# Optimization experiments

Measured on AMD Instinct MI355X. Metric: run time of the kernel, lower is better.

## Reference

```python
import jax, jax.numpy as jnp
import numpy as np

S, B, D_IN, HID, N_HEADS = 512, 64, 256, 512, 4


def setup_inputs() -> dict:
    key = jax.random.key(0)
    ks = jax.random.split(key, 16)
    din = D_IN + HID  # 768, gate linear fan-in
    sg = 1.0 / np.sqrt(din)
    sa = 1.0 / np.sqrt(HID)
    n = lambda k, shape, s: (jax.random.normal(k, shape, jnp.float32) * s)
    return {
        "x": jax.random.normal(ks[0], (S, B, D_IN), jnp.float32),
        # LSTM gate weights, stored (in, out) for x @ W + b
        "Wf": n(ks[1], (din, HID), sg), "bf": n(ks[2], (HID,), sg),
        "Wi": n(ks[3], (din, HID), sg), "bi": n(ks[4], (HID,), sg),
        "Wg": n(ks[5], (din, HID), sg), "bg": n(ks[6], (HID,), sg),
        "Wo": n(ks[7], (din, HID), sg), "bo": n(ks[8], (HID,), sg),
        # attention projections (out_proj unused in original forward, omitted)
        "Wq": n(ks[9], (HID, HID), sa), "bq": n(ks[10], (HID,), sa),
        "Wk": n(ks[11], (HID, HID), sa), "bk": n(ks[12], (HID,), sa),
        "Wv": n(ks[13], (HID, HID), sa), "bv": n(ks[14], (HID,), sa),
    }


def _forward(x, Wf, bf, Wi, bi, Wg, bg, Wo, bo, Wq, bq, Wk, bk, Wv, bv):
    Sl, Bs, _ = x.shape
    h0 = jnp.zeros((Bs, HID), x.dtype)
    c0 = jnp.zeros((Bs, HID), x.dtype)

    def step(carry, xt):
        hx, cx = carry
        comb = jnp.concatenate([xt, hx], axis=1)  # [B, D_IN+HID]
        f = jax.nn.sigmoid(comb @ Wf + bf)
        i = jax.nn.sigmoid(comb @ Wi + bi)
        g = jnp.tanh(comb @ Wg + bg)
        o = jax.nn.sigmoid(comb @ Wo + bo)
        cx = f * cx + i * g
        hx = o * jnp.tanh(cx)
        return (hx, cx), hx

    (hx, cx), lstm_out = jax.lax.scan(step, (h0, c0), x)  # lstm_out: [S, B, HID]

    dk = HID // N_HEADS
    # Faithful to original quirk: view (S,B,E) linear output as (B,S,H,dk) without transposing
    def proj(W, b):
        return (lstm_out @ W + b).reshape(Bs, Sl, N_HEADS, dk).transpose(0, 2, 1, 3)

    q, k, v = proj(Wq, bq), proj(Wk, bk), proj(Wv, bv)  # [B, H, S, dk]
    scores = jnp.einsum('bhqd,bhkd->bhqk', q, k) / np.sqrt(dk)
    attn = jax.nn.softmax(scores, axis=-1)
    out = jnp.einsum('bhqk,bhkd->bhqd', attn, v)  # [B, H, S, dk]
    out = out.transpose(0, 2, 1, 3).reshape(Bs, Sl, HID)
    decoded = jnp.swapaxes(out, 0, 1)  # [S, B, HID]
    return decoded, hx, cx


def reference(x, Wf, bf, Wi, bi, Wg, bg, Wo, bo, Wq, bq, Wk, bk, Wv, bv):
    return _forward(x, Wf, bf, Wi, bi, Wg, bg, Wo, bo, Wq, bq, Wk, bk, Wv, bv)
```

## Files before the change

### kernel.cpp

```cpp
#include <hip/hip_runtime.h>
#include <hip/hip_bf16.h>

typedef __attribute__((ext_vector_type(8))) short s8;
typedef __attribute__((ext_vector_type(4))) float f4;

using bf16 = __hip_bfloat16;

#define MFMA16(a,b,c) __builtin_amdgcn_mfma_f32_16x16x32_bf16((a),(b),(c),0,0,0)

constexpr int SS = 512, BBATCH = 64, HIDN = 512;
constexpr size_t DEC_SZ = (size_t)SS * BBATCH * HIDN;

constexpr size_t OF_FLAGS = 0;
constexpr size_t OF_BIAS4 = 65536;
constexpr size_t OF_BIASQ = 73728;
constexpr size_t OF_BTX   = 131072;
constexpr size_t OF_BTH   = 1179648;
constexpr size_t OF_BTQKV = 3276800;
constexpr size_t OF_YQ    = (size_t)5  << 20;
constexpr size_t OF_YK    = OF_YQ + ((size_t)32 << 20);
constexpr size_t OF_VT    = OF_YK + ((size_t)32 << 20);

constexpr size_t DOUT_LOUT = 0;
constexpr size_t DOUT_XBF  = (size_t)32 << 20;

__device__ inline s8 ldg8(const bf16* p){ return *(const s8*)p; }
__device__ inline short f2bs(float f){ return __builtin_bit_cast(short, __float2bfloat16(f)); }
__device__ inline float sigf(float x){ return 1.f/(1.f + __expf(-x)); }
__device__ inline float tanhf_(float x){ x = fminf(fmaxf(x, -15.f), 15.f); float e = __expf(2.f*x); return (e-1.f)/(e+1.f); }

__global__ void k0_pack(const float* x,
                        const float* Wf,const float* Wi,const float* Wg,const float* Wo,
                        const float* bfv,const float* biv,const float* bgv,const float* bov,
                        const float* Wq,const float* Wk,const float* Wv,
                        const float* bqv,const float* bkv,const float* bvv,
                        bf16* xbf, bf16* btx, bf16* bth, bf16* btqkv,
                        float* bias4, float* biasq, int* flags)
{
  const float* WG[4] = {Wf, Wi, Wg, Wo};
  const float* BG[4] = {bfv, biv, bgv, bov};
  const float* WQ[3] = {Wq, Wk, Wv};
  const float* BQ[3] = {bqv, bkv, bvv};
  const long NX   = 8388608;
  const long NBTH = 1048576;
  const long NBTQ = 786432;
  const long NBTX = 524288;
  const long NF   = 16384;
  const long TOT  = NX + NBTH + NBTQ + NBTX + NF + 2048 + 1536;
  long stride = (long)gridDim.x * blockDim.x;
  for (long i = (long)blockIdx.x*blockDim.x + threadIdx.x; i < TOT; i += stride){
    if (i < NX){ xbf[i] = __float2bfloat16(x[i]); }
    else if (i < NX + NBTH){
      long j = i - NX; int n = (int)(j >> 9), k = (int)(j & 511);
      int g = n >> 9, hid = n & 511;
      bth[j] = __float2bfloat16(WG[g][(size_t)(256 + k)*512 + hid]);
    } else if (i < NX + NBTH + NBTQ){
      long j = i - NX - NBTH; int n = (int)(j >> 9), k = (int)(j & 511);
      int w = n >> 9, c = n & 511;
      btqkv[j] = __float2bfloat16(WQ[w][(size_t)k*512 + c]);
    } else if (i < NX + NBTH + NBTQ + NBTX){
      long j = i - NX - NBTH - NBTQ; int n = (int)(j >> 8), k = (int)(j & 255);
      int g = n >> 9, hid = n & 511;
      btx[j] = __float2bfloat16(WG[g][(size_t)k*512 + hid]);
    } else if (i < NX + NBTH + NBTQ + NBTX + NF){
      flags[i - NX - NBTH - NBTQ - NBTX] = 0;
    } else if (i < NX + NBTH + NBTQ + NBTX + NF + 2048){
      long j = i - NX - NBTH - NBTQ - NBTX - NF; int g = (int)(j >> 9), hid = (int)(j & 511);
      bias4[j] = BG[g][hid];
    } else {
      long j = i - NX - NBTH - NBTQ - NBTX - NF - 2048; int w = (int)(j >> 9), c = (int)(j & 511);
      biasq[j] = BQ[w][c];
    }
  }
}

__global__ __launch_bounds__(512) void k1_lstm(const bf16* xbf, const bf16* btx, const bf16* bth,
                                               const float* bias4, bf16* lout, int* flags,
                                               float* out_tail)
{
  int ns = blockIdx.x;
  int tid = threadIdx.x, w = tid >> 6, lane = tid & 63;
  int mt = w >> 1, nh = w & 1, lm = lane & 15, q = lane >> 4;
  __shared__ float pre[64][68];
  s8 Bh[2][16], Bx[2][8];
  #pragma unroll
  for (int i = 0; i < 2; ++i){
    const bf16* bph = bth + ((size_t)((2*nh+i)*512 + ns*16 + lm)) * 512;
    #pragma unroll
    for (int kk = 0; kk < 16; ++kk) Bh[i][kk] = ldg8(bph + kk*32 + q*8);
    const bf16* bpx = btx + ((size_t)((2*nh+i)*512 + ns*16 + lm)) * 256;
    #pragma unroll
    for (int kk = 0; kk < 8; ++kk) Bx[i][kk] = ldg8(bpx + kk*32 + q*8);
  }
  int c0 = 2*tid, b0 = c0 >> 4, j0 = c0 & 15;
  float bs[8];
  #pragma unroll
  for (int g = 0; g < 4; ++g){
    bs[g]   = bias4[g*512 + ns*16 + j0];
    bs[4+g] = bias4[g*512 + ns*16 + j0 + 1];
  }
  float cs0 = 0.f, cs1 = 0.f;
  int budget = 1 << 22;

  for (int t = 0; t < 512; ++t){
    f4 acc[2] = {{0,0,0,0},{0,0,0,0}};
    const bf16* xr = xbf + ((size_t)(t*64 + mt*16 + lm)) * 256;
    #pragma unroll
    for (int kk = 0; kk < 8; ++kk){
      s8 A = ldg8(xr + kk*32 + q*8);
      acc[0] = MFMA16(A, Bx[0][kk], acc[0]);
      acc[1] = MFMA16(A, Bx[1][kk], acc[1]);
    }
    if (t > 0){
      int* fb = flags + (size_t)(t-1)*32;
      while (budget > 0){
        int v = 1;
        if (lane < 32) v = __hip_atomic_load(fb + lane, __ATOMIC_RELAXED, __HIP_MEMORY_SCOPE_AGENT);
        if (__ballot(v != 0) == ~0ull) break;
        budget--;
        __builtin_amdgcn_s_sleep(1);
      }
      __builtin_amdgcn_fence(__ATOMIC_ACQUIRE, "agent");
      const bf16* hr = lout + ((size_t)((t-1)*64 + mt*16 + lm)) * 512;
      #pragma unroll
      for (int kk = 0; kk < 16; ++kk){
        s8 A = ldg8(hr + kk*32 + q*8);
        acc[0] = MFMA16(A, Bh[0][kk], acc[0]);
        acc[1] = MFMA16(A, Bh[1][kk], acc[1]);
      }
    }
    #pragma unroll
    for (int i = 0; i < 2; ++i){
      int col = (2*nh+i)*16 + lm;
      #pragma unroll
      for (int r = 0; r < 4; ++r) pre[mt*16 + q*4 + r][col] = acc[i][r];
    }
    __syncthreads();
    {
      float fh0 = pre[b0][ 0+j0] + bs[0], fh1 = pre[b0][ 0+j0+1] + bs[4];
      float ih0 = pre[b0][16+j0] + bs[1], ih1 = pre[b0][16+j0+1] + bs[5];
      float gh0 = pre[b0][32+j0] + bs[2], gh1 = pre[b0][32+j0+1] + bs[6];
      float oh0 = pre[b0][48+j0] + bs[3], oh1 = pre[b0][48+j0+1] + bs[7];
      cs0 = sigf(fh0)*cs0 + sigf(ih0)*tanhf_(gh0);
      cs1 = sigf(fh1)*cs1 + sigf(ih1)*tanhf_(gh1);
      float h0 = sigf(oh0)*tanhf_(cs0);
      float h1 = sigf(oh1)*tanhf_(cs1);
      unsigned hv = (unsigned)(unsigned short)f2bs(h0) | ((unsigned)(unsigned short)f2bs(h1) << 16);
      __hip_atomic_store((unsigned*)(lout + ((size_t)(t*64 + b0))*512 + ns*16 + j0),
                         hv, __ATOMIC_RELAXED, __HIP_MEMORY_SCOPE_AGENT);
      if (t == 511){
        float* hx = out_tail + (size_t)b0*512 + ns*16 + j0;
        hx[0] = h0; hx[1] = h1;
        float* cx = out_tail + 32768 + (size_t)b0*512 + ns*16 + j0;
        cx[0] = cs0; cx[1] = cs1;
      }
    }
    __syncthreads();
    if (tid == 0)
      __hip_atomic_store(flags + (size_t)t*32 + ns, 1, __ATOMIC_RELEASE, __HIP_MEMORY_SCOPE_AGENT);
  }
}

__global__ __launch_bounds__(512) void k2_qkv(const bf16* lout, const bf16* btqkv, const float* biasq,
                                              bf16* yq, bf16* yk, bf16* vt)
{
  int nb = blockIdx.x, rb = blockIdx.y;
  int tid = threadIdx.x, w = tid >> 6, lane = tid & 63;
  int mt = w >> 1, nh = w & 1, lm = lane & 15, q = lane >> 4;
  int row = rb*64 + mt*16 + lm;
  f4 acc[2] = {{0,0,0,0},{0,0,0,0}};
  const bf16* ap  = lout + (size_t)row * 512;
  const bf16* bp0 = btqkv + ((size_t)(nb*64 + (2*nh+0)*16 + lm)) * 512;
  const bf16* bp1 = btqkv + ((size_t)(nb*64 + (2*nh+1)*16 + lm)) * 512;
  #pragma unroll
  for (int kk = 0; kk < 16; ++kk){
    int kb = kk*32 + q*8;
    s8 A = ldg8(ap + kb);
    acc[0] = MFMA16(A, ldg8(bp0 + kb), acc[0]);
    acc[1] = MFMA16(A, ldg8(bp1 + kb), acc[1]);
  }
  #pragma unroll
  for (int i = 0; i < 2; ++i){
    int e = nb*64 + (2*nh+i)*16 + lm;
    float bias = biasq[e];
    #pragma unroll
    for (int r = 0; r < 4; ++r){
      int rr = rb*64 + mt*16 + q*4 + r;
      bf16 v = __float2bfloat16(acc[i][r] + bias);
      if (e < 512)        yq[(size_t)rr*512 + e] = v;
      else if (e < 1024)  yk[(size_t)rr*512 + (e-512)] = v;
      else {
        int d = e - 1024, hh = d >> 7, dh = d & 127;
        vt[((size_t)((rr >> 9)*4 + hh)*128 + dh)*512 + (rr & 511)] = v;
      }
    }
  }
}

__global__ __launch_bounds__(256) void k3_attn(const bf16* yq, const bf16* yk, const bf16* vt,
                                               float* dec)
{
  int rb = blockIdx.x, bh = blockIdx.y;
  int b1 = bh >> 2, hh = bh & 3;
  int tid = threadIdx.x, w = tid >> 6, lane = tid & 63, lm = lane & 15, q = lane >> 4;
  __shared__ short sbuf[32768];
  short (*sK)[128] = (short(*)[128])sbuf;
  s8 Af[4];
  const bf16* apr = yq + ((size_t)(b1*512 + rb*64 + w*16 + lm))*512 + hh*128;
  #pragma unroll
  for (int kk = 0; kk < 4; ++kk) Af[kk] = ldg8(apr + kk*32 + q*8);
  f4 acc[32];
  #pragma unroll
  for (int nt = 0; nt < 32; ++nt) acc[nt] = (f4){0,0,0,0};

  for (int ch = 0; ch < 4; ++ch){
    __syncthreads();
    #pragma unroll
    for (int it = 0; it < 8; ++it){
      int lin = tid + it*256;
      int srow = lin >> 4, seg = lin & 15;
      int pseg = seg ^ (srow & 15);
      *(s8*)&sK[srow][pseg*8] =
        ldg8(yk + ((size_t)(b1*512 + ch*128 + srow))*512 + hh*128 + seg*8);
    }
    __syncthreads();
    #pragma unroll
    for (int ntl = 0; ntl < 8; ++ntl){
      int nt = ch*8 + ntl;
      int brow = ntl*16 + lm;
      #pragma unroll
      for (int kk = 0; kk < 4; ++kk){
        int c = (kk*4 + q) ^ lm;
        s8 Bfr = *(const s8*)&sK[brow][c*8];
        acc[nt] = MFMA16(Af[kk], Bfr, acc[nt]);
      }
    }
  }
  const float scale = 0.08838834764831845f;
  float mx[4], sm[4];
  #pragma unroll
  for (int r = 0; r < 4; ++r){
    float m = -1e30f;
    #pragma unroll
    for (int nt = 0; nt < 32; ++nt) m = fmaxf(m, acc[nt][r]);
    mx[r] = m;
  }
  #pragma unroll
  for (int d = 1; d < 16; d <<= 1){
    #pragma unroll
    for (int r = 0; r < 4; ++r) mx[r] = fmaxf(mx[r], __shfl_xor(mx[r], d, 64));
  }
  #pragma unroll
  for (int r = 0; r < 4; ++r){
    float s = 0.f;
    #pragma unroll
    for (int nt = 0; nt < 32; ++nt){
      float e = __expf(scale * (acc[nt][r] - mx[r]));
      acc[nt][r] = e; s += e;
    }
    sm[r] = s;
  }
  #pragma unroll
  for (int d = 1; d < 16; d <<= 1){
    #pragma unroll
    for (int r = 0; r < 4; ++r) sm[r] += __shfl_xor(sm[r], d, 64);
  }
  float inv[4];
  #pragma unroll
  for (int r = 0; r < 4; ++r) inv[r] = 1.f / sm[r];

  __syncthreads();
  #pragma unroll
  for (int nt = 0; nt < 32; ++nt){
    #pragma unroll
    for (int r = 0; r < 4; ++r){
      int rowp = w*16 + q*4 + r, col = nt*16 + lm;
      sbuf[rowp*512 + (((col >> 3) ^ (rowp & 15))*8) + (col & 7)] =
        f2bs(acc[nt][r] * inv[r]);
    }
  }
  f4 o[8];
  #pragma unroll
  for (int n2 = 0; n2 < 8; ++n2) o[n2] = (f4){0,0,0,0};
  int rowa = w*16 + lm;
  #pragma unroll
  for (int kk = 0; kk < 16; ++kk){
    s8 A = *(const s8*)&sbuf[rowa*512 + (((kk*4 + q) ^ (rowa & 15))*8)];
    #pragma unroll
    for (int n2 = 0; n2 < 8; ++n2){
      s8 Bfr = ldg8(vt + ((size_t)(bh*128 + n2*16 + lm))*512 + kk*32 + q*8);
      o[n2] = MFMA16(A, Bfr, o[n2]);
    }
  }
  #pragma unroll
  for (int n2 = 0; n2 < 8; ++n2){
    int d = n2*16 + lm;
    #pragma unroll
    for (int r = 0; r < 4; ++r){
      int s1 = rb*64 + w*16 + q*4 + r;
      dec[((size_t)s1*64 + b1)*512 + hh*128 + d] = o[n2][r];
    }
  }
}

extern "C" void kernel_launch(void* const* d_in, const int* in_sizes, int n_in,
                              void* d_out, int out_size, void* d_ws, size_t ws_size,
                              hipStream_t stream)
{
  const float* x   = (const float*)d_in[0];
  const float* Wf  = (const float*)d_in[1];  const float* bfv = (const float*)d_in[2];
  const float* Wi  = (const float*)d_in[3];  const float* biv = (const float*)d_in[4];
  const float* Wg  = (const float*)d_in[5];  const float* bgv = (const float*)d_in[6];
  const float* Wo  = (const float*)d_in[7];  const float* bov = (const float*)d_in[8];
  const float* Wq  = (const float*)d_in[9];  const float* bqv = (const float*)d_in[10];
  const float* Wk  = (const float*)d_in[11]; const float* bkv = (const float*)d_in[12];
  const float* Wv  = (const float*)d_in[13]; const float* bvv = (const float*)d_in[14];

  char* ws = (char*)d_ws;
  int*   flags = (int*)  (ws + OF_FLAGS);
  float* bias4 = (float*)(ws + OF_BIAS4);
  float* biasq = (float*)(ws + OF_BIASQ);
  bf16*  btx   = (bf16*) (ws + OF_BTX);
  bf16*  bth   = (bf16*) (ws + OF_BTH);
  bf16*  btqkv = (bf16*) (ws + OF_BTQKV);
  bf16*  yq    = (bf16*) (ws + OF_YQ);
  bf16*  yk    = (bf16*) (ws + OF_YK);
  bf16*  vt    = (bf16*) (ws + OF_VT);

  char* outc = (char*)d_out;
  bf16*  lout = (bf16*)(outc + DOUT_LOUT);
  bf16*  xbf  = (bf16*)(outc + DOUT_XBF);
  float* out  = (float*)d_out;

  hipLaunchKernelGGL(k0_pack, dim3(2048), dim3(256), 0, stream,
                     x, Wf, Wi, Wg, Wo, bfv, biv, bgv, bov, Wq, Wk, Wv, bqv, bkv, bvv,
                     xbf, btx, bth, btqkv, bias4, biasq, flags);
  hipLaunchKernelGGL(k1_lstm, dim3(32), dim3(512), 0, stream,
                     xbf, btx, bth, bias4, lout, flags, out + DEC_SZ);
  hipLaunchKernelGGL(k2_qkv, dim3(24, 512), dim3(512), 0, stream, lout, btqkv, biasq, yq, yk, vt);
  hipLaunchKernelGGL(k3_attn, dim3(8, 256), dim3(256), 0, stream, yq, yk, vt, out);
}
```

Baseline: 4.996 ms.

## Pin LSTM recurrence blocks to a single XCD and relax cross-block sync

Launches 512 LSTM blocks but keeps only the 32 that land on XCC 0, handing out slice indices through an atomic claim counter. All cooperating blocks then share one L2, so flag polling uses sc0 loads, h and flag stores become plain or volatile stores, and the acquire fence drops to workgroup scope. This aims to cut the per-timestep cross-XCD coherence latency in the serial recurrence. It relies on the hardware XCC register and on same-XCD L2 coherence, and it spends launch overhead on blocks that exit immediately.

```diff
diff --git a/kernel.cpp b/kernel.cpp
--- a/kernel.cpp
+++ b/kernel.cpp
@@ -7,6 +7,8 @@
 using bf16 = __hip_bfloat16;
 
 #define MFMA16(a,b,c) __builtin_amdgcn_mfma_f32_16x16x32_bf16((a),(b),(c),0,0,0)
+
+#define GETREG_XCC_ID (20 | (0 << 6) | (3 << 11))
 
 constexpr int SS = 512, BBATCH = 64, HIDN = 512;
 constexpr size_t DEC_SZ = (size_t)SS * BBATCH * HIDN;
@@ -14,6 +16,7 @@
 constexpr size_t OF_FLAGS = 0;
 constexpr size_t OF_BIAS4 = 65536;
 constexpr size_t OF_BIASQ = 73728;
+constexpr size_t OF_CLAIM = 81920;
 constexpr size_t OF_BTX   = 131072;
 constexpr size_t OF_BTH   = 1179648;
 constexpr size_t OF_BTQKV = 3276800;
@@ -35,7 +38,7 @@
                         const float* Wq,const float* Wk,const float* Wv,
                         const float* bqv,const float* bkv,const float* bvv,
                         bf16* xbf, bf16* btx, bf16* bth, bf16* btqkv,
-                        float* bias4, float* biasq, int* flags)
+                        float* bias4, float* biasq, int* flags, int* claim)
 {
   const float* WG[4] = {Wf, Wi, Wg, Wo};
   const float* BG[4] = {bfv, biv, bgv, bov};
@@ -46,7 +49,7 @@
   const long NBTQ = 786432;
   const long NBTX = 524288;
   const long NF   = 16384;
-  const long TOT  = NX + NBTH + NBTQ + NBTX + NF + 2048 + 1536;
+  const long TOT  = NX + NBTH + NBTQ + NBTX + NF + 2048 + 1536 + 1;
   long stride = (long)gridDim.x * blockDim.x;
   for (long i = (long)blockIdx.x*blockDim.x + threadIdx.x; i < TOT; i += stride){
     if (i < NX){ xbf[i] = __float2bfloat16(x[i]); }
@@ -67,18 +70,33 @@
     } else if (i < NX + NBTH + NBTQ + NBTX + NF + 2048){
       long j = i - NX - NBTH - NBTQ - NBTX - NF; int g = (int)(j >> 9), hid = (int)(j & 511);
       bias4[j] = BG[g][hid];
-    } else {
+    } else if (i < NX + NBTH + NBTQ + NBTX + NF + 2048 + 1536){
       long j = i - NX - NBTH - NBTQ - NBTX - NF - 2048; int w = (int)(j >> 9), c = (int)(j & 511);
       biasq[j] = BQ[w][c];
+    } else {
+      claim[0] = 0;
     }
   }
 }
 
 __global__ __launch_bounds__(512) void k1_lstm(const bf16* xbf, const bf16* btx, const bf16* bth,
                                                const float* bias4, bf16* lout, int* flags,
-                                               float* out_tail)
-{
-  int ns = blockIdx.x;
+                                               int* claim, float* out_tail)
+{
+  __shared__ int s_ns;
+  int xcc = (int)(__builtin_amdgcn_s_getreg(GETREG_XCC_ID) & 15);
+  if (threadIdx.x == 0){
+    int nsl = -1;
+    if (xcc == 0){
+      nsl = __hip_atomic_fetch_add(claim, 1, __ATOMIC_RELAXED, __HIP_MEMORY_SCOPE_AGENT);
+      if (nsl >= 32) nsl = -1;
+    }
+    s_ns = nsl;
+  }
+  __syncthreads();
+  int ns = s_ns;
+  if (ns < 0) return;
+
   int tid = threadIdx.x, w = tid >> 6, lane = tid & 63;
   int mt = w >> 1, nh = w & 1, lm = lane & 15, q = lane >> 4;
   __shared__ float pre[64][68];
@@ -100,7 +118,7 @@
     bs[4+g] = bias4[g*512 + ns*16 + j0 + 1];
   }
   float cs0 = 0.f, cs1 = 0.f;
-  int budget = 1 << 22;
+  int budget = 1 << 20;
 
   for (int t = 0; t < 512; ++t){
     f4 acc[2] = {{0,0,0,0},{0,0,0,0}};
@@ -112,15 +130,16 @@
       acc[1] = MFMA16(A, Bx[1][kk], acc[1]);
     }
     if (t > 0){
-      int* fb = flags + (size_t)(t-1)*32;
+      const int* fp = flags + (size_t)(t-1)*32 + (lane & 31);
       while (budget > 0){
-        int v = 1;
-        if (lane < 32) v = __hip_atomic_load(fb + lane, __ATOMIC_RELAXED, __HIP_MEMORY_SCOPE_AGENT);
-        if (__ballot(v != 0) == ~0ull) break;
+        int v;
+        asm volatile("global_load_dword %0, %1, off sc0\n\ts_waitcnt vmcnt(0)"
+                     : "=v"(v) : "v"(fp) : "memory");
+        if (__ballot(v != 0 || lane >= 32) == ~0ull) break;
         budget--;
         __builtin_amdgcn_s_sleep(1);
       }
-      __builtin_amdgcn_fence(__ATOMIC_ACQUIRE, "agent");
+      __builtin_amdgcn_fence(__ATOMIC_ACQUIRE, "workgroup");
       const bf16* hr = lout + ((size_t)((t-1)*64 + mt*16 + lm)) * 512;
       #pragma unroll
       for (int kk = 0; kk < 16; ++kk){
@@ -146,8 +165,7 @@
       float h0 = sigf(oh0)*tanhf_(cs0);
       float h1 = sigf(oh1)*tanhf_(cs1);
       unsigned hv = (unsigned)(unsigned short)f2bs(h0) | ((unsigned)(unsigned short)f2bs(h1) << 16);
-      __hip_atomic_store((unsigned*)(lout + ((size_t)(t*64 + b0))*512 + ns*16 + j0),
-                         hv, __ATOMIC_RELAXED, __HIP_MEMORY_SCOPE_AGENT);
+      *(unsigned*)(lout + ((size_t)(t*64 + b0))*512 + ns*16 + j0) = hv;
       if (t == 511){
         float* hx = out_tail + (size_t)b0*512 + ns*16 + j0;
         hx[0] = h0; hx[1] = h1;
@@ -157,7 +175,7 @@
     }
     __syncthreads();
     if (tid == 0)
-      __hip_atomic_store(flags + (size_t)t*32 + ns, 1, __ATOMIC_RELEASE, __HIP_MEMORY_SCOPE_AGENT);
+      *(volatile int*)(flags + (size_t)t*32 + ns) = 1;
   }
 }
 
@@ -320,6 +338,7 @@
   int*   flags = (int*)  (ws + OF_FLAGS);
   float* bias4 = (float*)(ws + OF_BIAS4);
   float* biasq = (float*)(ws + OF_BIASQ);
+  int*   claim = (int*)  (ws + OF_CLAIM);
   bf16*  btx   = (bf16*) (ws + OF_BTX);
   bf16*  bth   = (bf16*) (ws + OF_BTH);
   bf16*  btqkv = (bf16*) (ws + OF_BTQKV);
@@ -334,9 +353,9 @@
 
   hipLaunchKernelGGL(k0_pack, dim3(2048), dim3(256), 0, stream,
                      x, Wf, Wi, Wg, Wo, bfv, biv, bgv, bov, Wq, Wk, Wv, bqv, bkv, bvv,
-                     xbf, btx, bth, btqkv, bias4, biasq, flags);
-  hipLaunchKernelGGL(k1_lstm, dim3(32), dim3(512), 0, stream,
-                     xbf, btx, bth, bias4, lout, flags, out + DEC_SZ);
+                     xbf, btx, bth, btqkv, bias4, biasq, flags, claim);
+  hipLaunchKernelGGL(k1_lstm, dim3(512), dim3(512), 0, stream,
+                     xbf, btx, bth, bias4, lout, flags, claim, out + DEC_SZ);
   hipLaunchKernelGGL(k2_qkv, dim3(24, 512), dim3(512), 0, stream, lout, btqkv, biasq, yq, yk, vt);
   hipLaunchKernelGGL(k3_attn, dim3(8, 256), dim3(256), 0, stream, yq, yk, vt, out);
 }
```

Result: faster. 4.332 ms (-13.3%).
